# Kernel optimization log

Hardware: AMD Instinct MI355X
Metric: run time of the kernel (lower is better)

## Reference

```python
import jax, jax.numpy as jnp
import numpy as np

N_NODES = 10000
W_DIM = 512
N_EDGES = 200000


def setup_inputs() -> dict:
    key = jax.random.key(0)
    k1, k2, k3 = jax.random.split(key, 3)
    z_drug = jax.random.normal(k1, (N_NODES, W_DIM), dtype=jnp.float32)
    # glorot-style init for the bilinear weight
    glorot_std = jnp.sqrt(2.0 / (W_DIM + W_DIM)).astype(jnp.float32)
    weight = jax.random.normal(k2, (W_DIM, W_DIM), dtype=jnp.float32) * glorot_std
    batch_edges = jax.random.randint(k3, (2, N_EDGES), 0, N_NODES, dtype=jnp.int64)
    return {"z_drug": z_drug, "weight": weight, "batch_edges": batch_edges}


def reference(z_drug, weight, batch_edges):
    # edge_type == 'drug_drug': both endpoints come from the drug table.
    row_embed = z_drug[batch_edges[0]]  # [E, d]
    col_embed = z_drug[batch_edges[1]]  # [E, d]
    # score_e = row_e @ W @ col_e  == diag((Z1 W) Z2^T) without the N x N blowup
    score = jnp.einsum('ed,df,ef->e', row_embed, weight, col_embed)
    return jax.nn.sigmoid(score)  # is_sigmoid=True default
```

## Files before the change

kernel.cpp:

```cpp
#include <hip/hip_runtime.h>
#include <math.h>

#define DIM     512
#define NNODES  10000
#define NEDGES  200000
#define MPAD    10240
#define NMB     160
#define GEMM_GRID (NMB * 4)

using floatx4 = __attribute__((ext_vector_type(4))) float;
using half8   = __attribute__((ext_vector_type(8))) _Float16;
using half2v  = __attribute__((ext_vector_type(2))) _Float16;

template <int N> struct IC { static constexpr int v = N; };

__device__ inline float dot2acc(half2v a, half2v b, float c) {
#if __has_builtin(__builtin_amdgcn_fdot2)
    return __builtin_amdgcn_fdot2(a, b, c, false);
#else
    return fmaf((float)a[0], (float)b[0], fmaf((float)a[1], (float)b[1], c));
#endif
}

#define PREP_ZBLK 2560
#define PREP_GRID (PREP_ZBLK + 64)
__global__ __launch_bounds__(256) void prep(const float* __restrict__ Z,
                                            const float* __restrict__ W,
                                            _Float16* __restrict__ Zh16,
                                            _Float16* __restrict__ Wh16t) {
    const int b = blockIdx.x;
    const int t = threadIdx.x;

    if (b < PREP_ZBLK) {
        const int idx8 = (b * 256 + t) * 8;
        const int m = idx8 >> 9;
        float x[8];
        if (m < NNODES) {
            float4 v0 = *(const float4*)(Z + idx8);
            float4 v1 = *(const float4*)(Z + idx8 + 4);
            x[0]=v0.x; x[1]=v0.y; x[2]=v0.z; x[3]=v0.w;
            x[4]=v1.x; x[5]=v1.y; x[6]=v1.z; x[7]=v1.w;
        } else {
            #pragma unroll
            for (int j = 0; j < 8; ++j) x[j] = 0.f;
        }
        half8 h;
        #pragma unroll
        for (int j = 0; j < 8; ++j) h[j] = (_Float16)x[j];
        *(half8*)(Zh16 + idx8) = h;
    } else {
        __shared__ float tile[64][65];
        const int wb = b - PREP_ZBLK;
        const int kb = (wb >> 3) * 64;
        const int nb = (wb & 7) * 64;
        const int kk = t >> 2;
        const int ch = t & 3;

        const float* src = W + (size_t)(kb + kk) * DIM + nb + ch * 16;
        #pragma unroll
        for (int q = 0; q < 4; ++q) {
            float4 v = *(const float4*)(src + q * 4);
            tile[kk][ch * 16 + q * 4 + 0] = v.x;
            tile[kk][ch * 16 + q * 4 + 1] = v.y;
            tile[kk][ch * 16 + q * 4 + 2] = v.z;
            tile[kk][ch * 16 + q * 4 + 3] = v.w;
        }
        __syncthreads();

        const int nn = kk;
        half8 h0, h1;
        #pragma unroll
        for (int i = 0; i < 8; ++i) h0[i] = (_Float16)tile[ch * 16 + i][nn];
        #pragma unroll
        for (int i = 0; i < 8; ++i) h1[i] = (_Float16)tile[ch * 16 + 8 + i][nn];
        _Float16* d = Wh16t + (size_t)(nb + nn) * DIM + kb + ch * 16;
        *(half8*)(d)     = h0;
        *(half8*)(d + 8) = h1;
    }
}

__global__ __launch_bounds__(256, 3) void gemm_f16(
        const _Float16* __restrict__ Zh16,
        const _Float16* __restrict__ Wh16t,
        _Float16* __restrict__ ZWh)
{
    __shared__ _Float16 Abuf[2][2 * 64 * 32];
    __shared__ _Float16 Bbuf[2][2 * 128 * 32];

    const int t   = threadIdx.x;
    const int bid = blockIdx.x;

    const int cxd = bid & 7;
    const int rr  = bid >> 3;
    const int mg  = (rr >> 2) * 8 + cxd;
    const int m0  = mg * 64;
    const int n0  = (rr & 3) * 128;

    const int l  = t & 63;
    const int w  = t >> 6;
    const int wn = w * 32;
    const int lm = l & 15;
    const int lq = l >> 4;
    const unsigned wbase = (unsigned)(t & 192);

    floatx4 acc[4][2] = {};

    auto stage = [&](int buf, int k0) {
        #pragma unroll
        for (int p = 0; p < 2; ++p) {
            const int s   = p * 256 + t;
            const int kk  = s >> 8;
            const int row = (s >> 2) & 63;
            const int ch  = s & 3;
            const _Float16* src = Zh16 + (size_t)(m0 + row) * DIM + k0 + kk * 32 + ch * 8;
            __builtin_amdgcn_global_load_lds(
                (const __attribute__((address_space(1))) void*)src,
                (__attribute__((address_space(3))) void*)&Abuf[buf][(p * 256 + wbase) * 8],
                16, 0, 0);
        }
        #pragma unroll
        for (int p = 0; p < 4; ++p) {
            const int s   = p * 256 + t;
            const int kk  = s >> 9;
            const int row = (s >> 2) & 127;
            const int ch  = s & 3;
            const _Float16* src = Wh16t + (size_t)(n0 + row) * DIM + k0 + kk * 32 + ch * 8;
            __builtin_amdgcn_global_load_lds(
                (const __attribute__((address_space(1))) void*)src,
                (__attribute__((address_space(3))) void*)&Bbuf[buf][(p * 256 + wbase) * 8],
                16, 0, 0);
        }
    };

    stage(0, 0);
    stage(1, 64);

    auto step = [&](auto Sc) {
        constexpr int S   = decltype(Sc)::v;
        constexpr int buf = S & 1;
        if constexpr (S < 7) asm volatile("s_waitcnt vmcnt(6)" ::: "memory");
        else                 asm volatile("s_waitcnt vmcnt(0)" ::: "memory");
        __builtin_amdgcn_sched_barrier(0);
        __builtin_amdgcn_s_barrier();
        __builtin_amdgcn_sched_barrier(0);

        half8 aF[2][4], bF[2][2];
        #pragma unroll
        for (int kk = 0; kk < 2; ++kk) {
            #pragma unroll
            for (int i = 0; i < 4; ++i)
                aF[kk][i] = *(const half8*)&Abuf[buf][kk * 2048 + (16 * i + lm) * 32 + lq * 8];
            #pragma unroll
            for (int j = 0; j < 2; ++j)
                bF[kk][j] = *(const half8*)&Bbuf[buf][kk * 4096 + (wn + 16 * j + lm) * 32 + lq * 8];
        }
        asm volatile("s_waitcnt lgkmcnt(0)" ::: "memory");
        __builtin_amdgcn_sched_barrier(0);
        __builtin_amdgcn_s_barrier();
        __builtin_amdgcn_sched_barrier(0);

        if constexpr (S < 6) stage(buf, (S + 2) * 64);

        #pragma unroll
        for (int kk = 0; kk < 2; ++kk)
            #pragma unroll
            for (int i = 0; i < 4; ++i)
                #pragma unroll
                for (int j = 0; j < 2; ++j)
                    acc[i][j] = __builtin_amdgcn_mfma_f32_16x16x32_f16(
                        aF[kk][i], bF[kk][j], acc[i][j], 0, 0, 0);
    };

    step(IC<0>{}); step(IC<1>{}); step(IC<2>{}); step(IC<3>{});
    step(IC<4>{}); step(IC<5>{}); step(IC<6>{}); step(IC<7>{});

    #pragma unroll
    for (int i = 0; i < 4; ++i)
        #pragma unroll
        for (int j = 0; j < 2; ++j)
            #pragma unroll
            for (int r = 0; r < 4; ++r) {
                const int gm = m0 + 16 * i + lq * 4 + r;
                const int gn = n0 + wn + 16 * j + lm;
                if (gm < NNODES)
                    ZWh[(size_t)gm * DIM + gn] = (_Float16)acc[i][j][r];
            }
}

__global__ __launch_bounds__(256) void edge_score_u(const _Float16* __restrict__ ZWh,
                                                    const _Float16* __restrict__ Zh,
                                                    const int* __restrict__ eidx,
                                                    float* __restrict__ out) {
    const int t    = threadIdx.x;
    const int lane = t & 63;
    const int gq   = lane >> 4;
    const int sl   = lane & 15;

    const int e = blockIdx.x * 16 + (t >> 6) * 4 + gq;
    const int r = eidx[e];
    const int c = eidx[NEDGES + e];

    const _Float16* rp = ZWh + (size_t)r * DIM + sl * 32;
    const _Float16* cp = Zh  + (size_t)c * DIM + sl * 32;

    half8 ra0 = *(const half8*)(rp);
    half8 ra1 = *(const half8*)(rp + 8);
    half8 ra2 = *(const half8*)(rp + 16);
    half8 ra3 = *(const half8*)(rp + 24);
    half8 c0  = *(const half8*)(cp);
    half8 c1  = *(const half8*)(cp + 8);
    half8 c2  = *(const half8*)(cp + 16);
    half8 c3  = *(const half8*)(cp + 24);

    float s = 0.f;
    #pragma unroll
    for (int d = 0; d < 4; ++d) {
        s = dot2acc((half2v){ra0[2*d], ra0[2*d+1]}, (half2v){c0[2*d], c0[2*d+1]}, s);
        s = dot2acc((half2v){ra1[2*d], ra1[2*d+1]}, (half2v){c1[2*d], c1[2*d+1]}, s);
        s = dot2acc((half2v){ra2[2*d], ra2[2*d+1]}, (half2v){c2[2*d], c2[2*d+1]}, s);
        s = dot2acc((half2v){ra3[2*d], ra3[2*d+1]}, (half2v){c3[2*d], c3[2*d+1]}, s);
    }

    s += __shfl_xor(s, 1, 64);
    s += __shfl_xor(s, 2, 64);
    s += __shfl_xor(s, 4, 64);
    s += __shfl_xor(s, 8, 64);

    if (sl == 0)
        out[e] = 1.0f / (1.0f + expf(-s));
}

#define GTM 128
#define GTN 64
#define GTK 16
#define LDA 132
#define LDB 68

__global__ __launch_bounds__(256) void gemm_zw(const float* __restrict__ A,
                                               const float* __restrict__ B,
                                               float* __restrict__ C) {
    __shared__ float As[GTK * LDA];
    __shared__ float Bs[GTK * LDB];

    const int t  = threadIdx.x;
    const int m0 = blockIdx.x * GTM;
    const int n0 = blockIdx.y * GTN;
    const int tx = t & 15;
    const int ty = t >> 4;

    float acc[8][4] = {};

    for (int k0 = 0; k0 < DIM; k0 += GTK) {
        #pragma unroll
        for (int p = 0; p < 2; ++p) {
            int f  = t + p * 256;
            int mm = f >> 2;
            int kq = f & 3;
            int m  = m0 + mm;
            float4 v = make_float4(0.f, 0.f, 0.f, 0.f);
            if (m < NNODES)
                v = *(const float4*)(A + (size_t)m * DIM + k0 + kq * 4);
            As[(kq * 4 + 0) * LDA + mm] = v.x;
            As[(kq * 4 + 1) * LDA + mm] = v.y;
            As[(kq * 4 + 2) * LDA + mm] = v.z;
            As[(kq * 4 + 3) * LDA + mm] = v.w;
        }
        {
            int kb = t >> 4, n4 = t & 15;
            *(float4*)&Bs[kb * LDB + n4 * 4] =
                *(const float4*)(B + (size_t)(k0 + kb) * DIM + n0 + n4 * 4);
        }
        __syncthreads();

        #pragma unroll
        for (int kk = 0; kk < GTK; ++kk) {
            float4 a0 = *(const float4*)&As[kk * LDA + ty * 8];
            float4 a1 = *(const float4*)&As[kk * LDA + ty * 8 + 4];
            float4 b  = *(const float4*)&Bs[kk * LDB + tx * 4];
            float av[8] = {a0.x, a0.y, a0.z, a0.w, a1.x, a1.y, a1.z, a1.w};
            float bv[4] = {b.x, b.y, b.z, b.w};
            #pragma unroll
            for (int i = 0; i < 8; ++i)
                #pragma unroll
                for (int j = 0; j < 4; ++j)
                    acc[i][j] = fmaf(av[i], bv[j], acc[i][j]);
        }
        __syncthreads();
    }

    #pragma unroll
    for (int i = 0; i < 8; ++i) {
        int m = m0 + ty * 8 + i;
        if (m < NNODES)
            *(float4*)(C + (size_t)m * DIM + n0 + tx * 4) =
                make_float4(acc[i][0], acc[i][1], acc[i][2], acc[i][3]);
    }
}

__global__ __launch_bounds__(256) void edge_score(const float* __restrict__ ZW,
                                                  const float* __restrict__ Z,
                                                  const int* __restrict__ eidx,
                                                  float* __restrict__ out) {
    const int e    = blockIdx.x * 4 + (threadIdx.x >> 6);
    const int lane = threadIdx.x & 63;

    const int r = eidx[e];
    const int c = eidx[NEDGES + e];

    const float4* pr = (const float4*)(ZW + (size_t)r * DIM);
    const float4* pc = (const float4*)(Z  + (size_t)c * DIM);

    float4 a0 = pr[lane * 2 + 0];
    float4 a1 = pr[lane * 2 + 1];
    float4 b0 = pc[lane * 2 + 0];
    float4 b1 = pc[lane * 2 + 1];

    float s = a0.x * b0.x;
    s = fmaf(a0.y, b0.y, s);
    s = fmaf(a0.z, b0.z, s);
    s = fmaf(a0.w, b0.w, s);
    s = fmaf(a1.x, b1.x, s);
    s = fmaf(a1.y, b1.y, s);
    s = fmaf(a1.z, b1.z, s);
    s = fmaf(a1.w, b1.w, s);

    #pragma unroll
    for (int off = 32; off > 0; off >>= 1)
        s += __shfl_xor(s, off, 64);

    if (lane == 0)
        out[e] = 1.0f / (1.0f + expf(-s));
}

extern "C" void kernel_launch(void* const* d_in, const int* in_sizes, int n_in,
                              void* d_out, int out_size, void* d_ws, size_t ws_size,
                              hipStream_t stream) {
    const float* Z  = (const float*)d_in[0];
    const float* W  = (const float*)d_in[1];
    const int*   EI = (const int*)d_in[2];
    float* out = (float*)d_out;

    char* p = (char*)d_ws;
    _Float16* ZWh   = (_Float16*)p;  p += (size_t)MPAD * DIM * 2;
    _Float16* Zh16  = (_Float16*)p;  p += (size_t)MPAD * DIM * 2;
    _Float16* Wh16t = (_Float16*)p;  p += (size_t)DIM * DIM * 2;
    const size_t need_full = (size_t)(p - (char*)d_ws);

    if (ws_size >= need_full) {
        prep<<<PREP_GRID, 256, 0, stream>>>(Z, W, Zh16, Wh16t);
        gemm_f16<<<GEMM_GRID, 256, 0, stream>>>(Zh16, Wh16t, ZWh);
        edge_score_u<<<NEDGES / 16, 256, 0, stream>>>(ZWh, Zh16, EI, out);
    } else {
        float* ZW = (float*)d_ws;
        dim3 g1((NNODES + GTM - 1) / GTM, DIM / GTN);
        gemm_zw<<<g1, 256, 0, stream>>>(Z, W, ZW);
        edge_score<<<NEDGES / 4, 256, 0, stream>>>(ZW, Z, EI, out);
    }
}
```

Baseline: 128.8 us.

## Bucket-sort edges by column node inside the GEMM launch for gather locality

Extra blocks are added to the GEMM launch. They build a histogram of edge column indices in buckets of 64 nodes, scan it, and scatter packed (row, col, edge id) records into bucket order. Flag spin-waits order these phases, and the flags are zeroed in the prep kernel. The edge-score kernel then reads the sorted records, so edges that gather neighbouring Zh rows run close together, and it writes each score back to its original edge index. The aim is better L2 reuse on the column gathers, paid for with the sort work, an extra 1.6 MB of slot traffic, and a dependence on inter-block spin-waiting that assumes the histogram and scan blocks make progress.

```diff
diff --git a/kernel.cpp b/kernel.cpp
--- a/kernel.cpp
+++ b/kernel.cpp
@@ -7,10 +7,20 @@
 #define MPAD    10240
 #define NMB     160
 #define GEMM_GRID (NMB * 4)
+#define BKT     157
+
+#define HIST_BLK   64
+#define SCAN_BID   64
+#define SCAT_BASE  65
+#define SCAT_N     199
+#define GEMM_BASE  264
+#define FUSE_GRID  (GEMM_BASE + GEMM_GRID)
+#define ECHUNK     25000
 
 using floatx4 = __attribute__((ext_vector_type(4))) float;
 using half8   = __attribute__((ext_vector_type(8))) _Float16;
 using half2v  = __attribute__((ext_vector_type(2))) _Float16;
+typedef unsigned long long ull;
 
 template <int N> struct IC { static constexpr int v = N; };
 
@@ -22,14 +32,33 @@
 #endif
 }
 
+__device__ inline int aload(const int* p) {
+    return __hip_atomic_load(p, __ATOMIC_RELAXED, __HIP_MEMORY_SCOPE_AGENT);
+}
+__device__ inline void astore(int* p, int v) {
+    __hip_atomic_store(p, v, __ATOMIC_RELAXED, __HIP_MEMORY_SCOPE_AGENT);
+}
+__device__ inline void waitflag(int* f, int target) {
+    while (__hip_atomic_load(f, __ATOMIC_RELAXED, __HIP_MEMORY_SCOPE_AGENT) < target)
+        __builtin_amdgcn_s_sleep(8);
+    __atomic_signal_fence(__ATOMIC_ACQUIRE);
+}
+__device__ inline void signal(int* f) {
+    __atomic_signal_fence(__ATOMIC_RELEASE);
+    __hip_atomic_fetch_add(f, 1, __ATOMIC_RELAXED, __HIP_MEMORY_SCOPE_AGENT);
+}
+
 #define PREP_ZBLK 2560
 #define PREP_GRID (PREP_ZBLK + 64)
 __global__ __launch_bounds__(256) void prep(const float* __restrict__ Z,
                                             const float* __restrict__ W,
                                             _Float16* __restrict__ Zh16,
-                                            _Float16* __restrict__ Wh16t) {
+                                            _Float16* __restrict__ Wh16t,
+                                            int* __restrict__ counts) {
     const int b = blockIdx.x;
     const int t = threadIdx.x;
+
+    if (b == 0 && t < BKT + 4) counts[t] = 0;
 
     if (b < PREP_ZBLK) {
         const int idx8 = (b * 256 + t) * 8;
@@ -79,126 +108,205 @@
     }
 }
 
-__global__ __launch_bounds__(256, 3) void gemm_f16(
+__global__ __launch_bounds__(256, 3) void gemm_sort(
         const _Float16* __restrict__ Zh16,
         const _Float16* __restrict__ Wh16t,
-        _Float16* __restrict__ ZWh)
+        _Float16* __restrict__ ZWh,
+        const int* __restrict__ eidx,
+        int* __restrict__ counts,
+        int* __restrict__ cursor,
+        ull* __restrict__ slots,
+        int* __restrict__ flags)
 {
     __shared__ _Float16 Abuf[2][2 * 64 * 32];
     __shared__ _Float16 Bbuf[2][2 * 128 * 32];
+    __shared__ int s_cnt[BKT], s_base[BKT], s_off[BKT];
+    __shared__ int s_scan[256];
 
     const int t   = threadIdx.x;
     const int bid = blockIdx.x;
 
-    const int cxd = bid & 7;
-    const int rr  = bid >> 3;
-    const int mg  = (rr >> 2) * 8 + cxd;
-    const int m0  = mg * 64;
-    const int n0  = (rr & 3) * 128;
-
-    const int l  = t & 63;
-    const int w  = t >> 6;
-    const int wn = w * 32;
-    const int lm = l & 15;
-    const int lq = l >> 4;
-    const unsigned wbase = (unsigned)(t & 192);
-
-    floatx4 acc[4][2] = {};
-
-    auto stage = [&](int buf, int k0) {
-        #pragma unroll
-        for (int p = 0; p < 2; ++p) {
-            const int s   = p * 256 + t;
-            const int kk  = s >> 8;
-            const int row = (s >> 2) & 63;
-            const int ch  = s & 3;
-            const _Float16* src = Zh16 + (size_t)(m0 + row) * DIM + k0 + kk * 32 + ch * 8;
-            __builtin_amdgcn_global_load_lds(
-                (const __attribute__((address_space(1))) void*)src,
-                (__attribute__((address_space(3))) void*)&Abuf[buf][(p * 256 + wbase) * 8],
-                16, 0, 0);
-        }
-        #pragma unroll
-        for (int p = 0; p < 4; ++p) {
-            const int s   = p * 256 + t;
-            const int kk  = s >> 9;
-            const int row = (s >> 2) & 127;
-            const int ch  = s & 3;
-            const _Float16* src = Wh16t + (size_t)(n0 + row) * DIM + k0 + kk * 32 + ch * 8;
-            __builtin_amdgcn_global_load_lds(
-                (const __attribute__((address_space(1))) void*)src,
-                (__attribute__((address_space(3))) void*)&Bbuf[buf][(p * 256 + wbase) * 8],
-                16, 0, 0);
-        }
-    };
-
-    stage(0, 0);
-    stage(1, 64);
-
-    auto step = [&](auto Sc) {
-        constexpr int S   = decltype(Sc)::v;
-        constexpr int buf = S & 1;
-        if constexpr (S < 7) asm volatile("s_waitcnt vmcnt(6)" ::: "memory");
-        else                 asm volatile("s_waitcnt vmcnt(0)" ::: "memory");
-        __builtin_amdgcn_sched_barrier(0);
-        __builtin_amdgcn_s_barrier();
-        __builtin_amdgcn_sched_barrier(0);
-
-        half8 aF[2][4], bF[2][2];
-        #pragma unroll
-        for (int kk = 0; kk < 2; ++kk) {
-            #pragma unroll
-            for (int i = 0; i < 4; ++i)
-                aF[kk][i] = *(const half8*)&Abuf[buf][kk * 2048 + (16 * i + lm) * 32 + lq * 8];
-            #pragma unroll
-            for (int j = 0; j < 2; ++j)
-                bF[kk][j] = *(const half8*)&Bbuf[buf][kk * 4096 + (wn + 16 * j + lm) * 32 + lq * 8];
-        }
-        asm volatile("s_waitcnt lgkmcnt(0)" ::: "memory");
-        __builtin_amdgcn_sched_barrier(0);
-        __builtin_amdgcn_s_barrier();
-        __builtin_amdgcn_sched_barrier(0);
-
-        if constexpr (S < 6) stage(buf, (S + 2) * 64);
-
-        #pragma unroll
-        for (int kk = 0; kk < 2; ++kk)
-            #pragma unroll
-            for (int i = 0; i < 4; ++i)
+    if (bid >= GEMM_BASE) {
+        const int s8  = bid - GEMM_BASE;
+        const int cxd = bid & 7;
+        const int rr  = s8 >> 3;
+        const int mg  = (rr >> 2) * 8 + cxd;
+        const int m0  = mg * 64;
+        const int n0  = (rr & 3) * 128;
+
+        const int l  = t & 63;
+        const int w  = t >> 6;
+        const int wn = w * 32;
+        const int lm = l & 15;
+        const int lq = l >> 4;
+        const unsigned wbase = (unsigned)(t & 192);
+
+        floatx4 acc[4][2] = {};
+
+        auto stage = [&](int buf, int k0) {
+            #pragma unroll
+            for (int p = 0; p < 2; ++p) {
+                const int s   = p * 256 + t;
+                const int kk  = s >> 8;
+                const int row = (s >> 2) & 63;
+                const int ch  = s & 3;
+                const _Float16* src = Zh16 + (size_t)(m0 + row) * DIM + k0 + kk * 32 + ch * 8;
+                __builtin_amdgcn_global_load_lds(
+                    (const __attribute__((address_space(1))) void*)src,
+                    (__attribute__((address_space(3))) void*)&Abuf[buf][(p * 256 + wbase) * 8],
+                    16, 0, 0);
+            }
+            #pragma unroll
+            for (int p = 0; p < 4; ++p) {
+                const int s   = p * 256 + t;
+                const int kk  = s >> 9;
+                const int row = (s >> 2) & 127;
+                const int ch  = s & 3;
+                const _Float16* src = Wh16t + (size_t)(n0 + row) * DIM + k0 + kk * 32 + ch * 8;
+                __builtin_amdgcn_global_load_lds(
+                    (const __attribute__((address_space(1))) void*)src,
+                    (__attribute__((address_space(3))) void*)&Bbuf[buf][(p * 256 + wbase) * 8],
+                    16, 0, 0);
+            }
+        };
+
+        stage(0, 0);
+        stage(1, 64);
+
+        auto step = [&](auto Sc) {
+            constexpr int S   = decltype(Sc)::v;
+            constexpr int buf = S & 1;
+            if constexpr (S < 7) asm volatile("s_waitcnt vmcnt(6)" ::: "memory");
+            else                 asm volatile("s_waitcnt vmcnt(0)" ::: "memory");
+            __builtin_amdgcn_sched_barrier(0);
+            __builtin_amdgcn_s_barrier();
+            __builtin_amdgcn_sched_barrier(0);
+
+            half8 aF[2][4], bF[2][2];
+            #pragma unroll
+            for (int kk = 0; kk < 2; ++kk) {
+                #pragma unroll
+                for (int i = 0; i < 4; ++i)
+                    aF[kk][i] = *(const half8*)&Abuf[buf][kk * 2048 + (16 * i + lm) * 32 + lq * 8];
                 #pragma unroll
                 for (int j = 0; j < 2; ++j)
-                    acc[i][j] = __builtin_amdgcn_mfma_f32_16x16x32_f16(
-                        aF[kk][i], bF[kk][j], acc[i][j], 0, 0, 0);
-    };
-
-    step(IC<0>{}); step(IC<1>{}); step(IC<2>{}); step(IC<3>{});
-    step(IC<4>{}); step(IC<5>{}); step(IC<6>{}); step(IC<7>{});
-
-    #pragma unroll
-    for (int i = 0; i < 4; ++i)
-        #pragma unroll
-        for (int j = 0; j < 2; ++j)
-            #pragma unroll
-            for (int r = 0; r < 4; ++r) {
-                const int gm = m0 + 16 * i + lq * 4 + r;
-                const int gn = n0 + wn + 16 * j + lm;
-                if (gm < NNODES)
-                    ZWh[(size_t)gm * DIM + gn] = (_Float16)acc[i][j][r];
+                    bF[kk][j] = *(const half8*)&Bbuf[buf][kk * 4096 + (wn + 16 * j + lm) * 32 + lq * 8];
             }
-}
-
-__global__ __launch_bounds__(256) void edge_score_u(const _Float16* __restrict__ ZWh,
+            asm volatile("s_waitcnt lgkmcnt(0)" ::: "memory");
+            __builtin_amdgcn_sched_barrier(0);
+            __builtin_amdgcn_s_barrier();
+            __builtin_amdgcn_sched_barrier(0);
+
+            if constexpr (S < 6) stage(buf, (S + 2) * 64);
+
+            #pragma unroll
+            for (int kk = 0; kk < 2; ++kk)
+                #pragma unroll
+                for (int i = 0; i < 4; ++i)
+                    #pragma unroll
+                    for (int j = 0; j < 2; ++j)
+                        acc[i][j] = __builtin_amdgcn_mfma_f32_16x16x32_f16(
+                            aF[kk][i], bF[kk][j], acc[i][j], 0, 0, 0);
+        };
+
+        step(IC<0>{}); step(IC<1>{}); step(IC<2>{}); step(IC<3>{});
+        step(IC<4>{}); step(IC<5>{}); step(IC<6>{}); step(IC<7>{});
+
+        #pragma unroll
+        for (int i = 0; i < 4; ++i)
+            #pragma unroll
+            for (int j = 0; j < 2; ++j)
+                #pragma unroll
+                for (int r = 0; r < 4; ++r) {
+                    const int gm = m0 + 16 * i + lq * 4 + r;
+                    const int gn = n0 + wn + 16 * j + lm;
+                    if (gm < NNODES)
+                        ZWh[(size_t)gm * DIM + gn] = (_Float16)acc[i][j][r];
+                }
+        return;
+    }
+
+    if (bid < HIST_BLK) {
+        for (int i = t; i < BKT; i += 256) s_cnt[i] = 0;
+        __syncthreads();
+        for (int e = bid * 256 + t; e < NEDGES; e += HIST_BLK * 256)
+            atomicAdd(&s_cnt[eidx[NEDGES + e] >> 6], 1);
+        __syncthreads();
+        for (int i = t; i < BKT; i += 256)
+            if (s_cnt[i]) atomicAdd(&counts[i], s_cnt[i]);
+        __syncthreads();
+        if (t == 0) signal(&flags[0]);
+        return;
+    }
+
+    if (bid == SCAN_BID) {
+        if (t == 0) waitflag(&flags[0], HIST_BLK);
+        __syncthreads();
+        int v = (t < BKT) ? aload(counts + t) : 0;
+        s_scan[t] = v;
+        __syncthreads();
+        #pragma unroll
+        for (int off = 1; off < 256; off <<= 1) {
+            int u = (t >= off) ? s_scan[t - off] : 0;
+            __syncthreads();
+            s_scan[t] += u;
+            __syncthreads();
+        }
+        if (t < BKT) astore(cursor + t, s_scan[t] - v);
+        __syncthreads();
+        if (t == 0) signal(&flags[1]);
+        return;
+    }
+
+    {
+        const int sb = bid - SCAT_BASE;
+        for (int i = t; i < BKT; i += 256) { s_cnt[i] = 0; s_off[i] = 0; }
+        __syncthreads();
+        const int e0 = sb * 1024;
+        int myb[4];
+        #pragma unroll
+        for (int q = 0; q < 4; ++q) {
+            int e = e0 + q * 256 + t;
+            if (e < NEDGES) { myb[q] = eidx[NEDGES + e] >> 6; atomicAdd(&s_cnt[myb[q]], 1); }
+            else myb[q] = -1;
+        }
+        __syncthreads();
+        if (t == 0) waitflag(&flags[1], 1);
+        __syncthreads();
+        for (int i = t; i < BKT; i += 256)
+            if (s_cnt[i]) s_base[i] = atomicAdd(&cursor[i], s_cnt[i]);
+        __syncthreads();
+        #pragma unroll
+        for (int q = 0; q < 4; ++q)
+            if (myb[q] >= 0) {
+                int e = e0 + q * 256 + t;
+                int r = eidx[e];
+                int c = eidx[NEDGES + e];
+                int pos = s_base[myb[q]] + atomicAdd(&s_off[myb[q]], 1);
+                slots[pos] = ((ull)(unsigned)r << 32) |
+                             (ull)(((unsigned)c << 18) | (unsigned)e);
+            }
+    }
+}
+
+__global__ __launch_bounds__(256) void edge_score_b(const _Float16* __restrict__ ZWh,
                                                     const _Float16* __restrict__ Zh,
-                                                    const int* __restrict__ eidx,
+                                                    const ull* __restrict__ slots,
                                                     float* __restrict__ out) {
     const int t    = threadIdx.x;
     const int lane = t & 63;
     const int gq   = lane >> 4;
     const int sl   = lane & 15;
 
-    const int e = blockIdx.x * 16 + (t >> 6) * 4 + gq;
-    const int r = eidx[e];
-    const int c = eidx[NEDGES + e];
+    const int chunk = blockIdx.x & 7;
+    const int blk   = blockIdx.x >> 3;
+    const int ii    = chunk * ECHUNK + blk * 16 + (t >> 6) * 4 + gq;
+    if (ii >= (chunk + 1) * ECHUNK) return;
+
+    const ull  v = slots[ii];
+    const unsigned k = (unsigned)v;
+    const int c = (int)(k >> 18);
+    const int r = (int)((v >> 32) & 0xFFFFu);
 
     const _Float16* rp = ZWh + (size_t)r * DIM + sl * 32;
     const _Float16* cp = Zh  + (size_t)c * DIM + sl * 32;
@@ -227,7 +335,7 @@
     s += __shfl_xor(s, 8, 64);
 
     if (sl == 0)
-        out[e] = 1.0f / (1.0f + expf(-s));
+        out[k & 0x3FFFFu] = 1.0f / (1.0f + expf(-s));
 }
 
 #define GTM 128
@@ -344,12 +452,17 @@
     _Float16* ZWh   = (_Float16*)p;  p += (size_t)MPAD * DIM * 2;
     _Float16* Zh16  = (_Float16*)p;  p += (size_t)MPAD * DIM * 2;
     _Float16* Wh16t = (_Float16*)p;  p += (size_t)DIM * DIM * 2;
+    int* counts  = (int*)p;          p += (size_t)BKT * 4;
+    int* flags   = (int*)p;          p += 4 * 4;
+    int* cursor  = (int*)p;          p += (size_t)BKT * 4;
+    ull* slots   = (ull*)p;          p += (size_t)NEDGES * 8;
     const size_t need_full = (size_t)(p - (char*)d_ws);
 
     if (ws_size >= need_full) {
-        prep<<<PREP_GRID, 256, 0, stream>>>(Z, W, Zh16, Wh16t);
-        gemm_f16<<<GEMM_GRID, 256, 0, stream>>>(Zh16, Wh16t, ZWh);
-        edge_score_u<<<NEDGES / 16, 256, 0, stream>>>(ZWh, Zh16, EI, out);
+        prep<<<PREP_GRID, 256, 0, stream>>>(Z, W, Zh16, Wh16t, counts);
+        gemm_sort<<<FUSE_GRID, 256, 0, stream>>>(Zh16, Wh16t, ZWh, EI, counts,
+                                                 cursor, slots, flags);
+        edge_score_b<<<8 * ((ECHUNK + 15) / 16), 256, 0, stream>>>(ZWh, Zh16, slots, out);
     } else {
         float* ZW = (float*)d_ws;
         dim3 g1((NNODES + GTM - 1) / GTM, DIM / GTN);
```

Result: slower. 132.2 us (+2.6%).

## Bucket edges by row index and stage row tiles of ZW in LDS

Applied to the files above, without the earlier changes.

Adds histogram, scan and scatter kernels that group edges into buckets of 32 row nodes. The scoring kernel then loads each bucket's 32 ZW rows into shared memory once and reuses them for all edges in that bucket, so only the column embedding is gathered from global memory. The aim is to halve random-gather traffic in the edge kernel. In exchange it adds three small kernel launches, global atomics and an 8-byte-per-edge slot buffer, and bucket sizes may be uneven.

```diff
diff --git a/kernel.cpp b/kernel.cpp
--- a/kernel.cpp
+++ b/kernel.cpp
@@ -7,10 +7,14 @@
 #define MPAD    10240
 #define NMB     160
 #define GEMM_GRID (NMB * 4)
+#define BKT     313
+#define SPLIT   4
+#define ROWP    520
 
 using floatx4 = __attribute__((ext_vector_type(4))) float;
 using half8   = __attribute__((ext_vector_type(8))) _Float16;
 using half2v  = __attribute__((ext_vector_type(2))) _Float16;
+typedef unsigned long long ull;
 
 template <int N> struct IC { static constexpr int v = N; };
 
@@ -27,9 +31,15 @@
 __global__ __launch_bounds__(256) void prep(const float* __restrict__ Z,
                                             const float* __restrict__ W,
                                             _Float16* __restrict__ Zh16,
-                                            _Float16* __restrict__ Wh16t) {
+                                            _Float16* __restrict__ Wh16t,
+                                            int* __restrict__ counts) {
     const int b = blockIdx.x;
     const int t = threadIdx.x;
+
+    if (b == 0) {
+        if (t < BKT) counts[t] = 0;
+        if (t + 256 < BKT) counts[t + 256] = 0;
+    }
 
     if (b < PREP_ZBLK) {
         const int idx8 = (b * 256 + t) * 8;
@@ -79,6 +89,74 @@
     }
 }
 
+__global__ __launch_bounds__(256) void hist_k(const int* __restrict__ eidx,
+                                              int* __restrict__ counts) {
+    __shared__ int s_cnt[BKT];
+    const int t = threadIdx.x;
+    for (int i = t; i < BKT; i += 256) s_cnt[i] = 0;
+    __syncthreads();
+    for (int e = blockIdx.x * 256 + t; e < NEDGES; e += 64 * 256)
+        atomicAdd(&s_cnt[eidx[e] >> 5], 1);
+    __syncthreads();
+    for (int i = t; i < BKT; i += 256)
+        if (s_cnt[i]) atomicAdd(&counts[i], s_cnt[i]);
+}
+
+__global__ __launch_bounds__(512) void scan_k(const int* __restrict__ counts,
+                                              int* __restrict__ bstart,
+                                              int* __restrict__ cursor) {
+    __shared__ int s[512];
+    const int t = threadIdx.x;
+    int v = (t < BKT) ? counts[t] : 0;
+    s[t] = v;
+    __syncthreads();
+    #pragma unroll
+    for (int off = 1; off < 512; off <<= 1) {
+        int u = (t >= off) ? s[t - off] : 0;
+        __syncthreads();
+        s[t] += u;
+        __syncthreads();
+    }
+    if (t < BKT) {
+        const int ex = s[t] - v;
+        bstart[t] = ex;
+        cursor[t] = ex;
+    }
+    if (t == 0) bstart[BKT] = NEDGES;
+}
+
+#define SCAT_BLKS 196
+__global__ __launch_bounds__(256) void scatter_k(const int* __restrict__ eidx,
+                                                 int* __restrict__ cursor,
+                                                 ull* __restrict__ slots) {
+    __shared__ int s_cnt[BKT], s_base[BKT], s_off[BKT];
+    const int t = threadIdx.x;
+    for (int i = t; i < BKT; i += 256) { s_cnt[i] = 0; s_off[i] = 0; }
+    __syncthreads();
+    const int e0 = blockIdx.x * 1024;
+    int myb[4];
+    #pragma unroll
+    for (int q = 0; q < 4; ++q) {
+        int e = e0 + q * 256 + t;
+        if (e < NEDGES) { myb[q] = eidx[e] >> 5; atomicAdd(&s_cnt[myb[q]], 1); }
+        else myb[q] = -1;
+    }
+    __syncthreads();
+    for (int i = t; i < BKT; i += 256)
+        if (s_cnt[i]) s_base[i] = atomicAdd(&cursor[i], s_cnt[i]);
+    __syncthreads();
+    #pragma unroll
+    for (int q = 0; q < 4; ++q)
+        if (myb[q] >= 0) {
+            int e = e0 + q * 256 + t;
+            int r = eidx[e];
+            int c = eidx[NEDGES + e];
+            int pos = s_base[myb[q]] + atomicAdd(&s_off[myb[q]], 1);
+            slots[pos] = ((ull)(unsigned)r << 32) |
+                         (ull)(((unsigned)c << 18) | (unsigned)e);
+        }
+}
+
 __global__ __launch_bounds__(256, 3) void gemm_f16(
         const _Float16* __restrict__ Zh16,
         const _Float16* __restrict__ Wh16t,
@@ -187,47 +265,79 @@
             }
 }
 
-__global__ __launch_bounds__(256) void edge_score_u(const _Float16* __restrict__ ZWh,
+__global__ __launch_bounds__(256) void edge_score_s(const _Float16* __restrict__ ZWh,
                                                     const _Float16* __restrict__ Zh,
-                                                    const int* __restrict__ eidx,
+                                                    const ull* __restrict__ slots,
+                                                    const int* __restrict__ bstart,
                                                     float* __restrict__ out) {
-    const int t    = threadIdx.x;
-    const int lane = t & 63;
-    const int gq   = lane >> 4;
-    const int sl   = lane & 15;
-
-    const int e = blockIdx.x * 16 + (t >> 6) * 4 + gq;
-    const int r = eidx[e];
-    const int c = eidx[NEDGES + e];
-
-    const _Float16* rp = ZWh + (size_t)r * DIM + sl * 32;
-    const _Float16* cp = Zh  + (size_t)c * DIM + sl * 32;
-
-    half8 ra0 = *(const half8*)(rp);
-    half8 ra1 = *(const half8*)(rp + 8);
-    half8 ra2 = *(const half8*)(rp + 16);
-    half8 ra3 = *(const half8*)(rp + 24);
-    half8 c0  = *(const half8*)(cp);
-    half8 c1  = *(const half8*)(cp + 8);
-    half8 c2  = *(const half8*)(cp + 16);
-    half8 c3  = *(const half8*)(cp + 24);
-
-    float s = 0.f;
-    #pragma unroll
-    for (int d = 0; d < 4; ++d) {
-        s = dot2acc((half2v){ra0[2*d], ra0[2*d+1]}, (half2v){c0[2*d], c0[2*d+1]}, s);
-        s = dot2acc((half2v){ra1[2*d], ra1[2*d+1]}, (half2v){c1[2*d], c1[2*d+1]}, s);
-        s = dot2acc((half2v){ra2[2*d], ra2[2*d+1]}, (half2v){c2[2*d], c2[2*d+1]}, s);
-        s = dot2acc((half2v){ra3[2*d], ra3[2*d+1]}, (half2v){c3[2*d], c3[2*d+1]}, s);
-    }
-
-    s += __shfl_xor(s, 1, 64);
-    s += __shfl_xor(s, 2, 64);
-    s += __shfl_xor(s, 4, 64);
-    s += __shfl_xor(s, 8, 64);
-
-    if (sl == 0)
-        out[e] = 1.0f / (1.0f + expf(-s));
+    __shared__ _Float16 rows[32 * ROWP];
+
+    const int t   = threadIdx.x;
+    const int b   = blockIdx.x / SPLIT;
+    const int qtr = blockIdx.x % SPLIT;
+    const int r0  = b * 32;
+
+    #pragma unroll
+    for (int k = 0; k < 8; ++k) {
+        const int i   = t + k * 256;
+        const int row = i >> 6;
+        const int off = i & 63;
+        if (r0 + row < NNODES) {
+            half8 v = *(const half8*)(ZWh + (size_t)(r0 + row) * DIM + off * 8);
+            *(half8*)(rows + row * ROWP + off * 8) = v;
+        }
+    }
+    __syncthreads();
+
+    const int s0  = bstart[b];
+    const int s1  = bstart[b + 1];
+    const int len = s1 - s0;
+    const int q0  = s0 + (len * qtr) / SPLIT;
+    const int q1  = s0 + (len * (qtr + 1)) / SPLIT;
+
+    const int l  = t & 63;
+    const int w  = t >> 6;
+    const int gq = l >> 4;
+    const int sl = l & 15;
+
+    for (int base = q0; base < q1; base += 16) {
+        const int idx = base + w * 4 + gq;
+        float sa = 0.f, sb = 0.f;
+        int e = -1;
+        if (idx < q1) {
+            const ull v = slots[idx];
+            e = (int)(v & 0x3FFFFu);
+            const int c  = (int)((v >> 18) & 0x3FFFu);
+            const int rl = (int)(v >> 32) - r0;
+
+            const _Float16* rp = rows + rl * ROWP + sl * 32;
+            const _Float16* cp = Zh + (size_t)c * DIM + sl * 32;
+
+            half8 ra0 = *(const half8*)(rp);
+            half8 ra1 = *(const half8*)(rp + 8);
+            half8 ra2 = *(const half8*)(rp + 16);
+            half8 ra3 = *(const half8*)(rp + 24);
+            half8 c0  = *(const half8*)(cp);
+            half8 c1  = *(const half8*)(cp + 8);
+            half8 c2  = *(const half8*)(cp + 16);
+            half8 c3  = *(const half8*)(cp + 24);
+
+            #pragma unroll
+            for (int d = 0; d < 4; ++d) {
+                sa = dot2acc((half2v){ra0[2*d], ra0[2*d+1]}, (half2v){c0[2*d], c0[2*d+1]}, sa);
+                sb = dot2acc((half2v){ra1[2*d], ra1[2*d+1]}, (half2v){c1[2*d], c1[2*d+1]}, sb);
+                sa = dot2acc((half2v){ra2[2*d], ra2[2*d+1]}, (half2v){c2[2*d], c2[2*d+1]}, sa);
+                sb = dot2acc((half2v){ra3[2*d], ra3[2*d+1]}, (half2v){c3[2*d], c3[2*d+1]}, sb);
+            }
+        }
+        float s = sa + sb;
+        s += __shfl_xor(s, 1, 64);
+        s += __shfl_xor(s, 2, 64);
+        s += __shfl_xor(s, 4, 64);
+        s += __shfl_xor(s, 8, 64);
+        if (sl == 0 && e >= 0)
+            out[e] = 1.0f / (1.0f + expf(-s));
+    }
 }
 
 #define GTM 128
@@ -344,12 +454,19 @@
     _Float16* ZWh   = (_Float16*)p;  p += (size_t)MPAD * DIM * 2;
     _Float16* Zh16  = (_Float16*)p;  p += (size_t)MPAD * DIM * 2;
     _Float16* Wh16t = (_Float16*)p;  p += (size_t)DIM * DIM * 2;
+    int* counts  = (int*)p;          p += (size_t)BKT * 4;
+    int* bstart  = (int*)p;          p += (size_t)(BKT + 1) * 4;
+    int* cursor  = (int*)p;          p += (size_t)BKT * 4;
+    ull* slots   = (ull*)p;          p += (size_t)NEDGES * 8;
     const size_t need_full = (size_t)(p - (char*)d_ws);
 
     if (ws_size >= need_full) {
-        prep<<<PREP_GRID, 256, 0, stream>>>(Z, W, Zh16, Wh16t);
+        prep<<<PREP_GRID, 256, 0, stream>>>(Z, W, Zh16, Wh16t, counts);
+        hist_k<<<64, 256, 0, stream>>>(EI, counts);
+        scan_k<<<1, 512, 0, stream>>>(counts, bstart, cursor);
+        scatter_k<<<SCAT_BLKS, 256, 0, stream>>>(EI, cursor, slots);
         gemm_f16<<<GEMM_GRID, 256, 0, stream>>>(Zh16, Wh16t, ZWh);
-        edge_score_u<<<NEDGES / 16, 256, 0, stream>>>(ZWh, Zh16, EI, out);
+        edge_score_s<<<BKT * SPLIT, 256, 0, stream>>>(ZWh, Zh16, slots, bstart, out);
     } else {
         float* ZW = (float*)d_ws;
         dim3 g1((NNODES + GTM - 1) / GTM, DIM / GTN);
```

New measurement: 138.2 us. 1.07x slower.
